# Kernel tuning notes

Hardware: AMD Instinct MI355X
Metric: run time of the kernel (lower is better)

## Reference

```python
import jax, jax.numpy as jnp
import numpy as np

N, E, NB, P = 100000, 1600000, 1000, 500000


def gcn_conv(x, edge_index, W, b):
    # PyG GCNConv: add self-loops, symmetric D^-1/2 (A+I) D^-1/2 normalization,
    # linear transform, bias.
    n = x.shape[0]
    loop = jnp.arange(n, dtype=edge_index.dtype)
    src = jnp.concatenate([edge_index[0], loop])
    dst = jnp.concatenate([edge_index[1], loop])
    deg = jax.ops.segment_sum(jnp.ones(src.shape[0], x.dtype), dst, num_segments=n)
    dinv = jnp.where(deg > 0, jax.lax.rsqrt(deg), 0.0)
    norm = dinv[src] * dinv[dst]                       # [E+n]
    xw = x @ W                                          # [n, out]
    out = jax.ops.segment_sum(xw[src] * norm[:, None], dst, num_segments=n)
    return out + b


def setup_inputs() -> dict:
    key = jax.random.key(0)
    ks = jax.random.split(key, 12)
    x = jax.random.normal(ks[0], (N, 27), jnp.float32)
    edge_index = jax.random.randint(ks[1], (2, E), 0, N, dtype=jnp.int32)
    bank = jax.random.normal(ks[2], (NB, 27), jnp.float32)
    node1 = jax.random.randint(ks[3], (P,), 0, N + NB, dtype=jnp.int32)
    node2 = jax.random.randint(ks[4], (P,), 0, N + NB, dtype=jnp.int32)

    def lin(k, fan_in, fan_out):
        s = 1.0 / np.sqrt(fan_in)
        kw, kb = jax.random.split(k)
        W = jax.random.uniform(kw, (fan_in, fan_out), jnp.float32, -s, s)
        b = jax.random.uniform(kb, (fan_out,), jnp.float32, -s, s)
        return W, b

    W1, b1 = lin(ks[5], 27, 60)
    W2, b2 = lin(ks[6], 60, 50)
    Wb, bb = lin(ks[7], 27, 50)
    Wf1, bf1 = lin(ks[8], 100, 40)
    Wf2, bf2 = lin(ks[9], 40, 20)
    Wf3, bf3 = lin(ks[10], 20, 4)
    return dict(x=x, bank=bank, W1=W1, b1=b1, W2=W2, b2=b2, Wb=Wb, bb=bb,
                Wf1=Wf1, bf1=bf1, Wf2=Wf2, bf2=bf2, Wf3=Wf3, bf3=bf3,
                edge_index=edge_index, node1=node1, node2=node2)


def reference(x, bank, W1, b1, W2, b2, Wb, bb, Wf1, bf1, Wf2, bf2, Wf3, bf3,
              edge_index, node1, node2):
    h = gcn_conv(x, edge_index, W1, b1)                 # [N, 60]
    h = gcn_conv(h, edge_index, W2, b2)                 # [N, 50]
    bk = bank @ Wb + bb                                 # [NB, 50]
    allh = jnp.concatenate([h, bk], axis=0)             # [N+NB, 50]
    z = jnp.concatenate([allh[node1], allh[node2]], axis=1)  # [P, 100]
    z = z @ Wf1 + bf1
    z = z @ Wf2 + bf2
    z = z @ Wf3 + bf3                                   # [P, 4]
    return jax.nn.softmax(z, axis=0)                    # softmax over dim 0, as in source
```

## Files before the change

kernel.cpp:

```cpp
#include <hip/hip_runtime.h>
#include <math.h>

#define N_NODES 100000
#define N_EDGES 1600000
#define NB_BANK 1000
#define N_PAIRS 500000

#define BUCK_SHIFT 9
#define BUCK_NODES 512
#define NBUCK 196
#define EPB 16384
#define NSCAT 98
#define NZBLK 1954
#define SMASK 0x1FFFF

struct Consts {
  float C[27*8];
  float Rb[27*8];
  float u[8];
  float vg[8];
  float vb[8];
};

__global__ __launch_bounds__(256) void k_precompute(
    const float* __restrict__ W1, const float* __restrict__ b1,
    const float* __restrict__ W2, const float* __restrict__ b2,
    const float* __restrict__ Wb, const float* __restrict__ bb,
    const float* __restrict__ Wf1, const float* __restrict__ bf1,
    const float* __restrict__ Wf2, const float* __restrict__ bf2,
    const float* __restrict__ Wf3, const float* __restrict__ bf3,
    Consts* __restrict__ cst) {
  __shared__ float A[40*4];
  __shared__ float T[100*4];
  __shared__ float B[60*8];
  __shared__ float cvec[4];
  const int tid = threadIdx.x;

  for (int idx = tid; idx < 160; idx += 256) {
    int r = idx >> 2, k = idx & 3;
    float s = 0.f;
    for (int j = 0; j < 20; ++j) s += Wf2[r*20+j] * Wf3[j*4+k];
    A[idx] = s;
  }
  __syncthreads();
  for (int idx = tid; idx < 400; idx += 256) {
    int r = idx >> 2, k = idx & 3;
    float s = 0.f;
    for (int j = 0; j < 40; ++j) s += Wf1[r*40+j] * A[j*4+k];
    T[idx] = s;
  }
  if (tid < 4) {
    float s = bf3[tid];
    for (int j = 0; j < 40; ++j) s += bf1[j] * A[j*4+tid];
    for (int j = 0; j < 20; ++j) s += bf2[j] * Wf3[j*4+tid];
    cvec[tid] = s;
  }
  __syncthreads();
  for (int idx = tid; idx < 480; idx += 256) {
    int r = idx >> 3, k = idx & 7;
    int half = k >> 2, kk = k & 3;
    float s = 0.f;
    for (int j = 0; j < 50; ++j) s += W2[r*50+j] * T[(half*50+j)*4+kk];
    B[idx] = s;
  }
  __syncthreads();
  for (int idx = tid; idx < 456; idx += 256) {
    if (idx < 216) {
      int r = idx >> 3, k = idx & 7;
      float s = 0.f;
      for (int j = 0; j < 60; ++j) s += W1[r*60+j] * B[j*8+k];
      cst->C[idx] = s;
    } else if (idx < 432) {
      int i2 = idx - 216;
      int r = i2 >> 3, k = i2 & 7, half = k >> 2, kk = k & 3;
      float s = 0.f;
      for (int j = 0; j < 50; ++j) s += Wb[r*50+j] * T[(half*50+j)*4+kk];
      cst->Rb[i2] = s;
    } else if (idx < 440) {
      int k = idx - 432;
      float s = 0.f;
      for (int j = 0; j < 60; ++j) s += b1[j] * B[j*8+k];
      cst->u[k] = s;
    } else if (idx < 448) {
      int k = idx - 440, half = k >> 2, kk = k & 3;
      float s = (half == 0) ? cvec[kk] : 0.f;
      for (int j = 0; j < 50; ++j) s += b2[j] * T[(half*50+j)*4+kk];
      cst->vg[k] = s;
    } else {
      int k = idx - 448, half = k >> 2, kk = k & 3;
      float s = (half == 0) ? cvec[kk] : 0.f;
      for (int j = 0; j < 50; ++j) s += bb[j] * T[(half*50+j)*4+kk];
      cst->vb[k] = s;
    }
  }
}

__global__ __launch_bounds__(1024) void k_bcount(const int* __restrict__ ei,
                                                 int* __restrict__ bcnt) {
  __shared__ int hist[NBUCK];
  const int t = threadIdx.x;
  if (t < NBUCK) hist[t] = 0;
  __syncthreads();
  const int e0 = blockIdx.x * EPB;
  for (int i = t; i < EPB; i += 1024) {
    int e = e0 + i;
    if (e < N_EDGES) atomicAdd(&hist[ei[N_EDGES + e] >> BUCK_SHIFT], 1);
  }
  __syncthreads();
  if (t < NBUCK && hist[t]) atomicAdd(&bcnt[t], hist[t]);
}

__global__ __launch_bounds__(256) void k_bscan(const int* __restrict__ bcnt,
                                               int* __restrict__ boff,
                                               int* __restrict__ bcursor) {
  __shared__ int sm[256];
  int t = threadIdx.x;
  int v = (t < NBUCK) ? bcnt[t] : 0;
  sm[t] = v;
  __syncthreads();
  for (int off = 1; off < 256; off <<= 1) {
    int u = (t >= off) ? sm[t - off] : 0;
    __syncthreads();
    sm[t] += u;
    __syncthreads();
  }
  if (t < NBUCK) { int ex = sm[t] - v; boff[t] = ex; bcursor[t] = ex; }
  if (t == 0) boff[NBUCK] = N_EDGES;
}

__global__ __launch_bounds__(1024) void k_bscatter(const int* __restrict__ ei,
                                                   int* __restrict__ bcursor,
                                                   int* __restrict__ ebuf) {
  __shared__ int hist[NBUCK];
  __shared__ int base[NBUCK];
  const int t = threadIdx.x;
  const int e0 = blockIdx.x * EPB;
  if (t < NBUCK) hist[t] = 0;
  __syncthreads();
  for (int i = t; i < EPB; i += 1024) {
    int e = e0 + i;
    if (e < N_EDGES) atomicAdd(&hist[ei[N_EDGES + e] >> BUCK_SHIFT], 1);
  }
  __syncthreads();
  if (t < NBUCK) {
    int h = hist[t];
    base[t] = h ? atomicAdd(&bcursor[t], h) : 0;
    hist[t] = 0;
  }
  __syncthreads();
  for (int i = t; i < EPB; i += 1024) {
    int e = e0 + i;
    if (e < N_EDGES) {
      int s = ei[e], d = ei[N_EDGES + e];
      int b = d >> BUCK_SHIFT;
      int pos = base[b] + atomicAdd(&hist[b], 1);
      ebuf[pos] = ((d & (BUCK_NODES - 1)) << 17) | s;
    }
  }
}

__global__ __launch_bounds__(512) void k_degdinv(const int* __restrict__ boff,
                                                 const int* __restrict__ ebuf,
                                                 float* __restrict__ dinv,
                                                 int* __restrict__ rowptr) {
  __shared__ int cnt[BUCK_NODES];
  const int b = blockIdx.x;
  const int t = threadIdx.x;
  cnt[t] = 0;
  __syncthreads();
  const int beg = boff[b], end = boff[b + 1];
  for (int j = beg + t; j < end; j += 512)
    atomicAdd(&cnt[ebuf[j] >> 17], 1);
  __syncthreads();
  int v = cnt[t];
  for (int off = 1; off < 512; off <<= 1) {
    int u = (t >= off) ? cnt[t - off] : 0;
    __syncthreads();
    cnt[t] += u;
    __syncthreads();
  }
  int node = (b << BUCK_SHIFT) + t;
  if (node <= N_NODES) rowptr[node == N_NODES ? N_NODES : node] = beg + cnt[t] - v;
  if (node < N_NODES) dinv[node] = rsqrtf((float)v + 1.0f);
}

__global__ __launch_bounds__(256) void k_bfill(const int* __restrict__ boff,
                                               const int* __restrict__ rowptr,
                                               const int* __restrict__ ebuf,
                                               int* __restrict__ csr) {
  __shared__ int lcur[BUCK_NODES];
  const int b = blockIdx.x;
  const int nbase = b << BUCK_SHIFT;
  const int t = threadIdx.x;
  for (int i = t; i < BUCK_NODES; i += 256) {
    int node = nbase + i;
    lcur[i] = (node < N_NODES) ? rowptr[node] : N_EDGES;
  }
  __syncthreads();
  const int beg = boff[b], end = boff[b + 1];
  for (int j = beg + t; j < end; j += 256) {
    int code = ebuf[j];
    int pos = atomicAdd(&lcur[code >> 17], 1);
    csr[pos] = code & SMASK;
  }
}

__global__ __launch_bounds__(256) void k_x8(const float* __restrict__ x,
                                            const float* __restrict__ dinv,
                                            const Consts* __restrict__ cst,
                                            float* __restrict__ Xs) {
  __shared__ float xs[32*27];
  const int tid = threadIdx.x;
  const int base = blockIdx.x * 32 * 27;
  for (int j = tid; j < 32*27; j += 256) {
    int g = base + j;
    xs[j] = (g < N_NODES*27) ? x[g] : 0.f;
  }
  __syncthreads();
  int li = tid >> 3, k = tid & 7;
  int node = blockIdx.x * 32 + li;
  if (node < N_NODES) {
    float s = 0.f;
    for (int c = 0; c < 27; ++c) s += xs[li*27+c] * cst->C[c*8+k];
    Xs[node*8+k] = s * dinv[node];
  }
}

__global__ __launch_bounds__(256) void k_gather1(const int* __restrict__ rowptr,
                                                 const int* __restrict__ csr,
                                                 const float* __restrict__ dinv,
                                                 const float2* __restrict__ Xs2,
                                                 float2* __restrict__ Ys2,
                                                 float* __restrict__ dvec) {
  int t = blockIdx.x * 256 + threadIdx.x;
  int d = t >> 2, q = t & 3;
  if (d >= N_NODES) return;
  const int beg = rowptr[d], end = rowptr[d + 1];
  const float nd = dinv[d];
  float2 self = Xs2[d*4 + q];
  float ax = self.x, ay = self.y;
  float dsum = nd;
  int j = beg;
  for (; j + 4 <= end; j += 4) {
    int s0 = csr[j], s1 = csr[j+1], s2 = csr[j+2], s3 = csr[j+3];
    float2 a0 = Xs2[s0*4+q], a1 = Xs2[s1*4+q], a2 = Xs2[s2*4+q], a3 = Xs2[s3*4+q];
    ax += (a0.x + a1.x) + (a2.x + a3.x);
    ay += (a0.y + a1.y) + (a2.y + a3.y);
    if (q == 0) dsum += (dinv[s0] + dinv[s1]) + (dinv[s2] + dinv[s3]);
  }
  for (; j < end; ++j) {
    int s = csr[j];
    float2 a = Xs2[s*4+q];
    ax += a.x; ay += a.y;
    if (q == 0) dsum += dinv[s];
  }
  float nn = nd * nd;
  Ys2[t] = make_float2(nn * ax, nn * ay);
  if (q == 0) dvec[d] = nd * dsum;
}

__global__ __launch_bounds__(256) void k_gather2g(const int* __restrict__ rowptr,
                                                  const int* __restrict__ csr,
                                                  const float* __restrict__ dinv,
                                                  const float2* __restrict__ Ys2,
                                                  const float* __restrict__ dvec,
                                                  const float* __restrict__ bank,
                                                  const Consts* __restrict__ cst,
                                                  float2* __restrict__ gall2) {
  int t = blockIdx.x * 256 + threadIdx.x;
  int d = t >> 2, q = t & 3;
  if (d >= N_NODES + NB_BANK) return;
  int c0 = 2*q, c1 = 2*q + 1;
  if (d >= N_NODES) {
    int bk = d - N_NODES;
    float sx = cst->vb[c0], sy = cst->vb[c1];
    for (int cc = 0; cc < 27; ++cc) {
      float bv = bank[bk*27+cc];
      sx += bv * cst->Rb[cc*8+c0];
      sy += bv * cst->Rb[cc*8+c1];
    }
    gall2[t] = make_float2(sx, sy);
    return;
  }
  const int beg = rowptr[d], end = rowptr[d + 1];
  float2 self = Ys2[d*4 + q];
  float ax = self.x, ay = self.y;
  int j = beg;
  for (; j + 4 <= end; j += 4) {
    int s0 = csr[j], s1 = csr[j+1], s2 = csr[j+2], s3 = csr[j+3];
    float2 a0 = Ys2[s0*4+q], a1 = Ys2[s1*4+q], a2 = Ys2[s2*4+q], a3 = Ys2[s3*4+q];
    ax += (a0.x + a1.x) + (a2.x + a3.x);
    ay += (a0.y + a1.y) + (a2.y + a3.y);
  }
  for (; j < end; ++j) {
    float2 a = Ys2[csr[j]*4+q];
    ax += a.x; ay += a.y;
  }
  float nd = dinv[d], dv = dvec[d];
  gall2[t] = make_float2(nd * ax + dv * cst->u[c0] + cst->vg[c0],
                         nd * ay + dv * cst->u[c1] + cst->vg[c1]);
}

__device__ inline void sm_merge(float4& m1, float4& s1,
                                const float4 m2, const float4 s2) {
  float4 M;
  M.x = fmaxf(m1.x, m2.x); M.y = fmaxf(m1.y, m2.y);
  M.z = fmaxf(m1.z, m2.z); M.w = fmaxf(m1.w, m2.w);
  s1.x = s1.x * expf(m1.x - M.x) + s2.x * expf(m2.x - M.x);
  s1.y = s1.y * expf(m1.y - M.y) + s2.y * expf(m2.y - M.y);
  s1.z = s1.z * expf(m1.z - M.z) + s2.z * expf(m2.z - M.z);
  s1.w = s1.w * expf(m1.w - M.w) + s2.w * expf(m2.w - M.w);
  m1 = M;
}

__global__ __launch_bounds__(256) void k_z(const int* __restrict__ node1,
                                           const int* __restrict__ node2,
                                           const float* __restrict__ gall,
                                           float* __restrict__ z,
                                           float4* __restrict__ bs_m,
                                           float4* __restrict__ bs_s) {
  int p = blockIdx.x * 256 + threadIdx.x;
  float4 m = make_float4(-1e30f, -1e30f, -1e30f, -1e30f);
  float4 s = make_float4(0.f, 0.f, 0.f, 0.f);
  if (p < N_PAIRS) {
    int n1 = node1[p], n2 = node2[p];
    const float4 a = *(const float4*)(gall + (size_t)n1*8);
    const float4 b = *(const float4*)(gall + (size_t)n2*8 + 4);
    float4 zv = make_float4(a.x+b.x, a.y+b.y, a.z+b.z, a.w+b.w);
    ((float4*)z)[p] = zv;
    m = zv; s = make_float4(1.f, 1.f, 1.f, 1.f);
  }
  __shared__ float4 lm[256], ls[256];
  lm[threadIdx.x] = m; ls[threadIdx.x] = s;
  __syncthreads();
  for (int st = 128; st > 0; st >>= 1) {
    if (threadIdx.x < st) {
      float4 mm = lm[threadIdx.x], ss = ls[threadIdx.x];
      sm_merge(mm, ss, lm[threadIdx.x + st], ls[threadIdx.x + st]);
      lm[threadIdx.x] = mm; ls[threadIdx.x] = ss;
    }
    __syncthreads();
  }
  if (threadIdx.x == 0) { bs_m[blockIdx.x] = lm[0]; bs_s[blockIdx.x] = ls[0]; }
}

__global__ __launch_bounds__(256) void k_comb(const float4* __restrict__ bs_m,
                                              const float4* __restrict__ bs_s,
                                              float* __restrict__ gms) {
  float4 m = make_float4(-1e30f, -1e30f, -1e30f, -1e30f);
  float4 s = make_float4(0.f, 0.f, 0.f, 0.f);
  for (int i = threadIdx.x; i < NZBLK; i += 256)
    sm_merge(m, s, bs_m[i], bs_s[i]);
  __shared__ float4 lm[256], ls[256];
  lm[threadIdx.x] = m; ls[threadIdx.x] = s;
  __syncthreads();
  for (int st = 128; st > 0; st >>= 1) {
    if (threadIdx.x < st) {
      float4 mm = lm[threadIdx.x], ss = ls[threadIdx.x];
      sm_merge(mm, ss, lm[threadIdx.x + st], ls[threadIdx.x + st]);
      lm[threadIdx.x] = mm; ls[threadIdx.x] = ss;
    }
    __syncthreads();
  }
  if (threadIdx.x == 0) {
    float4 M = lm[0], S = ls[0];
    gms[0] = M.x; gms[1] = M.y; gms[2] = M.z; gms[3] = M.w;
    gms[4] = S.x; gms[5] = S.y; gms[6] = S.z; gms[7] = S.w;
  }
}

__global__ __launch_bounds__(256) void k_final(const float* __restrict__ z,
                                               const float* __restrict__ gms,
                                               float* __restrict__ out) {
  int p = blockIdx.x * 256 + threadIdx.x;
  if (p < N_PAIRS) {
    float m0 = gms[0], m1 = gms[1], m2 = gms[2], m3 = gms[3];
    float i0 = 1.f / gms[4], i1 = 1.f / gms[5];
    float i2 = 1.f / gms[6], i3 = 1.f / gms[7];
    float4 zv = ((const float4*)z)[p];
    float4 o = make_float4(expf(zv.x - m0) * i0, expf(zv.y - m1) * i1,
                           expf(zv.z - m2) * i2, expf(zv.w - m3) * i3);
    ((float4*)out)[p] = o;
  }
}

extern "C" void kernel_launch(void* const* d_in, const int* in_sizes, int n_in,
                              void* d_out, int out_size, void* d_ws, size_t ws_size,
                              hipStream_t stream) {
  const float* x    = (const float*)d_in[0];
  const float* bank = (const float*)d_in[1];
  const float* W1   = (const float*)d_in[2];
  const float* b1   = (const float*)d_in[3];
  const float* W2   = (const float*)d_in[4];
  const float* b2   = (const float*)d_in[5];
  const float* Wb   = (const float*)d_in[6];
  const float* bb   = (const float*)d_in[7];
  const float* Wf1  = (const float*)d_in[8];
  const float* bf1  = (const float*)d_in[9];
  const float* Wf2  = (const float*)d_in[10];
  const float* bf2  = (const float*)d_in[11];
  const float* Wf3  = (const float*)d_in[12];
  const float* bf3  = (const float*)d_in[13];
  const int* ei     = (const int*)d_in[14];
  const int* node1  = (const int*)d_in[15];
  const int* node2  = (const int*)d_in[16];
  float* out = (float*)d_out;

  char* w = (char*)d_ws;
  size_t off = 0;
  auto take = [&](size_t bytes) -> char* {
    char* p = w + off;
    off = (off + bytes + 255) & ~(size_t)255;
    return p;
  };
  Consts* cst    = (Consts*)take(sizeof(Consts));
  int*    bcnt   = (int*)take(NBUCK * 4);
  int*    boff   = (int*)take((NBUCK + 1) * 4);
  int*    bcursor= (int*)take(NBUCK * 4);
  float*  dinv   = (float*)take(N_NODES * 4);
  int*    rowptr = (int*)take((N_NODES + 1) * 4);
  int*    csr    = (int*)take((size_t)N_EDGES * 4);
  float*  Xs     = (float*)take((size_t)N_NODES * 8 * 4);
  float*  Ys     = (float*)take((size_t)N_NODES * 8 * 4);
  float*  dvec   = (float*)take(N_NODES * 4);
  float*  gall   = (float*)take((size_t)(N_NODES + NB_BANK) * 8 * 4);
  char*   shreg  = take((size_t)N_PAIRS * 16);
  int*    ebuf   = (int*)shreg;
  float*  z      = (float*)shreg;
  float4* bs_m   = (float4*)take((size_t)NZBLK * 16);
  float4* bs_s   = (float4*)take((size_t)NZBLK * 16);
  float*  gms    = (float*)take(32);

  hipMemsetAsync(bcnt, 0, NBUCK * 4, stream);

  k_precompute<<<1, 256, 0, stream>>>(W1, b1, W2, b2, Wb, bb,
                                      Wf1, bf1, Wf2, bf2, Wf3, bf3, cst);
  k_bcount<<<NSCAT, 1024, 0, stream>>>(ei, bcnt);
  k_bscan<<<1, 256, 0, stream>>>(bcnt, boff, bcursor);
  k_bscatter<<<NSCAT, 1024, 0, stream>>>(ei, bcursor, ebuf);
  k_degdinv<<<NBUCK, 512, 0, stream>>>(boff, ebuf, dinv, rowptr);
  k_bfill<<<NBUCK, 256, 0, stream>>>(boff, rowptr, ebuf, csr);
  k_x8<<<(N_NODES + 31) / 32, 256, 0, stream>>>(x, dinv, cst, Xs);
  k_gather1<<<(N_NODES * 4 + 255) / 256, 256, 0, stream>>>(
      rowptr, csr, dinv, (const float2*)Xs, (float2*)Ys, dvec);
  k_gather2g<<<((N_NODES + NB_BANK) * 4 + 255) / 256, 256, 0, stream>>>(
      rowptr, csr, dinv, (const float2*)Ys, dvec, bank, cst, (float2*)gall);
  k_z<<<NZBLK, 256, 0, stream>>>(node1, node2, gall, z, bs_m, bs_s);
  k_comb<<<1, 256, 0, stream>>>(bs_m, bs_s, gms);
  k_final<<<NZBLK, 256, 0, stream>>>(z, gms, out);
}
```

Baseline: 234.9 us.

## Fuse small kernels to cut launch count and merge graph-build stages

Folds the weight precompute into an extra block of the bucket-count kernel. Merges degree/dinv, CSR fill and the x@C projection into one per-bucket kernel. Replaces the separate softmax-combine kernel with a last-block ticket reduction inside k_z. This drops four kernel launches and the global round trips for rowptr/dinv. The cost is a serialized 8-chunk projection loop per bucket block with only 196 blocks, and extra fences and atomics.

```diff
diff --git a/kernel.cpp b/kernel.cpp
--- a/kernel.cpp
+++ b/kernel.cpp
@@ -22,7 +22,7 @@
   float vb[8];
 };
 
-__global__ __launch_bounds__(256) void k_precompute(
+__device__ void precompute_body(
     const float* __restrict__ W1, const float* __restrict__ b1,
     const float* __restrict__ W2, const float* __restrict__ b2,
     const float* __restrict__ Wb, const float* __restrict__ bb,
@@ -35,15 +35,16 @@
   __shared__ float B[60*8];
   __shared__ float cvec[4];
   const int tid = threadIdx.x;
-
-  for (int idx = tid; idx < 160; idx += 256) {
+  const int nt = blockDim.x;
+
+  for (int idx = tid; idx < 160; idx += nt) {
     int r = idx >> 2, k = idx & 3;
     float s = 0.f;
     for (int j = 0; j < 20; ++j) s += Wf2[r*20+j] * Wf3[j*4+k];
     A[idx] = s;
   }
   __syncthreads();
-  for (int idx = tid; idx < 400; idx += 256) {
+  for (int idx = tid; idx < 400; idx += nt) {
     int r = idx >> 2, k = idx & 3;
     float s = 0.f;
     for (int j = 0; j < 40; ++j) s += Wf1[r*40+j] * A[j*4+k];
@@ -56,7 +57,7 @@
     cvec[tid] = s;
   }
   __syncthreads();
-  for (int idx = tid; idx < 480; idx += 256) {
+  for (int idx = tid; idx < 480; idx += nt) {
     int r = idx >> 3, k = idx & 7;
     int half = k >> 2, kk = k & 3;
     float s = 0.f;
@@ -64,7 +65,7 @@
     B[idx] = s;
   }
   __syncthreads();
-  for (int idx = tid; idx < 456; idx += 256) {
+  for (int idx = tid; idx < 456; idx += nt) {
     if (idx < 216) {
       int r = idx >> 3, k = idx & 7;
       float s = 0.f;
@@ -95,8 +96,19 @@
   }
 }
 
-__global__ __launch_bounds__(1024) void k_bcount(const int* __restrict__ ei,
-                                                 int* __restrict__ bcnt) {
+__global__ __launch_bounds__(1024) void k_bcount(
+    const int* __restrict__ ei, int* __restrict__ bcnt,
+    const float* __restrict__ W1, const float* __restrict__ b1,
+    const float* __restrict__ W2, const float* __restrict__ b2,
+    const float* __restrict__ Wb, const float* __restrict__ bb,
+    const float* __restrict__ Wf1, const float* __restrict__ bf1,
+    const float* __restrict__ Wf2, const float* __restrict__ bf2,
+    const float* __restrict__ Wf3, const float* __restrict__ bf3,
+    Consts* __restrict__ cst) {
+  if (blockIdx.x == NSCAT) {
+    precompute_body(W1, b1, W2, b2, Wb, bb, Wf1, bf1, Wf2, bf2, Wf3, bf3, cst);
+    return;
+  }
   __shared__ int hist[NBUCK];
   const int t = threadIdx.x;
   if (t < NBUCK) hist[t] = 0;
@@ -159,11 +171,18 @@
   }
 }
 
-__global__ __launch_bounds__(512) void k_degdinv(const int* __restrict__ boff,
-                                                 const int* __restrict__ ebuf,
-                                                 float* __restrict__ dinv,
-                                                 int* __restrict__ rowptr) {
+__global__ __launch_bounds__(512) void k_mega(const int* __restrict__ boff,
+                                              const int* __restrict__ ebuf,
+                                              const float* __restrict__ x,
+                                              const Consts* __restrict__ cst,
+                                              float* __restrict__ dinv,
+                                              int* __restrict__ rowptr,
+                                              int* __restrict__ csr,
+                                              float* __restrict__ Xs) {
   __shared__ int cnt[BUCK_NODES];
+  __shared__ int lcur[BUCK_NODES];
+  __shared__ float dnv[BUCK_NODES];
+  __shared__ float xs[64*27];
   const int b = blockIdx.x;
   const int t = threadIdx.x;
   cnt[t] = 0;
@@ -179,50 +198,36 @@
     cnt[t] += u;
     __syncthreads();
   }
-  int node = (b << BUCK_SHIFT) + t;
-  if (node <= N_NODES) rowptr[node == N_NODES ? N_NODES : node] = beg + cnt[t] - v;
-  if (node < N_NODES) dinv[node] = rsqrtf((float)v + 1.0f);
-}
-
-__global__ __launch_bounds__(256) void k_bfill(const int* __restrict__ boff,
-                                               const int* __restrict__ rowptr,
-                                               const int* __restrict__ ebuf,
-                                               int* __restrict__ csr) {
-  __shared__ int lcur[BUCK_NODES];
-  const int b = blockIdx.x;
-  const int nbase = b << BUCK_SHIFT;
-  const int t = threadIdx.x;
-  for (int i = t; i < BUCK_NODES; i += 256) {
-    int node = nbase + i;
-    lcur[i] = (node < N_NODES) ? rowptr[node] : N_EDGES;
-  }
-  __syncthreads();
-  const int beg = boff[b], end = boff[b + 1];
-  for (int j = beg + t; j < end; j += 256) {
+  const int node = (b << BUCK_SHIFT) + t;
+  const int excl = beg + cnt[t] - v;
+  lcur[t] = excl;
+  float nd = rsqrtf((float)v + 1.0f);
+  dnv[t] = nd;
+  if (node < N_NODES) { rowptr[node] = excl; dinv[node] = nd; }
+  if (node == N_NODES) rowptr[N_NODES] = excl;
+  __syncthreads();
+  for (int chunk = 0; chunk < 8; ++chunk) {
+    const int nb = chunk * 64;
+    const int gbase = ((b << BUCK_SHIFT) + nb) * 27;
+    for (int i = t; i < 64*27; i += 512) {
+      int g = gbase + i;
+      xs[i] = (g < N_NODES*27) ? x[g] : 0.f;
+    }
+    __syncthreads();
+    int li = t >> 3, k = t & 7;
+    int ln = nb + li;
+    int gnode = (b << BUCK_SHIFT) + ln;
+    if (gnode < N_NODES) {
+      float s = 0.f;
+      for (int c = 0; c < 27; ++c) s += xs[li*27+c] * cst->C[c*8+k];
+      Xs[(size_t)gnode*8 + k] = s * dnv[ln];
+    }
+    __syncthreads();
+  }
+  for (int j = beg + t; j < end; j += 512) {
     int code = ebuf[j];
     int pos = atomicAdd(&lcur[code >> 17], 1);
     csr[pos] = code & SMASK;
-  }
-}
-
-__global__ __launch_bounds__(256) void k_x8(const float* __restrict__ x,
-                                            const float* __restrict__ dinv,
-                                            const Consts* __restrict__ cst,
-                                            float* __restrict__ Xs) {
-  __shared__ float xs[32*27];
-  const int tid = threadIdx.x;
-  const int base = blockIdx.x * 32 * 27;
-  for (int j = tid; j < 32*27; j += 256) {
-    int g = base + j;
-    xs[j] = (g < N_NODES*27) ? x[g] : 0.f;
-  }
-  __syncthreads();
-  int li = tid >> 3, k = tid & 7;
-  int node = blockIdx.x * 32 + li;
-  if (node < N_NODES) {
-    float s = 0.f;
-    for (int c = 0; c < 27; ++c) s += xs[li*27+c] * cst->C[c*8+k];
-    Xs[node*8+k] = s * dinv[node];
   }
 }
 
@@ -318,7 +323,9 @@
                                            const float* __restrict__ gall,
                                            float* __restrict__ z,
                                            float4* __restrict__ bs_m,
-                                           float4* __restrict__ bs_s) {
+                                           float4* __restrict__ bs_s,
+                                           int* __restrict__ ticket,
+                                           float* __restrict__ gms) {
   int p = blockIdx.x * 256 + threadIdx.x;
   float4 m = make_float4(-1e30f, -1e30f, -1e30f, -1e30f);
   float4 s = make_float4(0.f, 0.f, 0.f, 0.f);
@@ -331,6 +338,7 @@
     m = zv; s = make_float4(1.f, 1.f, 1.f, 1.f);
   }
   __shared__ float4 lm[256], ls[256];
+  __shared__ bool amLast;
   lm[threadIdx.x] = m; ls[threadIdx.x] = s;
   __syncthreads();
   for (int st = 128; st > 0; st >>= 1) {
@@ -341,18 +349,20 @@
     }
     __syncthreads();
   }
-  if (threadIdx.x == 0) { bs_m[blockIdx.x] = lm[0]; bs_s[blockIdx.x] = ls[0]; }
-}
-
-__global__ __launch_bounds__(256) void k_comb(const float4* __restrict__ bs_m,
-                                              const float4* __restrict__ bs_s,
-                                              float* __restrict__ gms) {
-  float4 m = make_float4(-1e30f, -1e30f, -1e30f, -1e30f);
-  float4 s = make_float4(0.f, 0.f, 0.f, 0.f);
+  if (threadIdx.x == 0) {
+    bs_m[blockIdx.x] = lm[0]; bs_s[blockIdx.x] = ls[0];
+    __threadfence();
+    int prev = atomicAdd(ticket, 1);
+    amLast = (prev == (int)gridDim.x - 1);
+  }
+  __syncthreads();
+  if (!amLast) return;
+  __threadfence();
+  float4 cm = make_float4(-1e30f, -1e30f, -1e30f, -1e30f);
+  float4 cs = make_float4(0.f, 0.f, 0.f, 0.f);
   for (int i = threadIdx.x; i < NZBLK; i += 256)
-    sm_merge(m, s, bs_m[i], bs_s[i]);
-  __shared__ float4 lm[256], ls[256];
-  lm[threadIdx.x] = m; ls[threadIdx.x] = s;
+    sm_merge(cm, cs, bs_m[i], bs_s[i]);
+  lm[threadIdx.x] = cm; ls[threadIdx.x] = cs;
   __syncthreads();
   for (int st = 128; st > 0; st >>= 1) {
     if (threadIdx.x < st) {
@@ -414,7 +424,8 @@
     return p;
   };
   Consts* cst    = (Consts*)take(sizeof(Consts));
-  int*    bcnt   = (int*)take(NBUCK * 4);
+  int*    bcnt   = (int*)take((NBUCK + 1) * 4);
+  int*    ticket = bcnt + NBUCK;
   int*    boff   = (int*)take((NBUCK + 1) * 4);
   int*    bcursor= (int*)take(NBUCK * 4);
   float*  dinv   = (float*)take(N_NODES * 4);
@@ -431,21 +442,17 @@
   float4* bs_s   = (float4*)take((size_t)NZBLK * 16);
   float*  gms    = (float*)take(32);
 
-  hipMemsetAsync(bcnt, 0, NBUCK * 4, stream);
-
-  k_precompute<<<1, 256, 0, stream>>>(W1, b1, W2, b2, Wb, bb,
-                                      Wf1, bf1, Wf2, bf2, Wf3, bf3, cst);
-  k_bcount<<<NSCAT, 1024, 0, stream>>>(ei, bcnt);
+  hipMemsetAsync(bcnt, 0, (NBUCK + 1) * 4, stream);
+
+  k_bcount<<<NSCAT + 1, 1024, 0, stream>>>(ei, bcnt, W1, b1, W2, b2, Wb, bb,
+                                           Wf1, bf1, Wf2, bf2, Wf3, bf3, cst);
   k_bscan<<<1, 256, 0, stream>>>(bcnt, boff, bcursor);
   k_bscatter<<<NSCAT, 1024, 0, stream>>>(ei, bcursor, ebuf);
-  k_degdinv<<<NBUCK, 512, 0, stream>>>(boff, ebuf, dinv, rowptr);
-  k_bfill<<<NBUCK, 256, 0, stream>>>(boff, rowptr, ebuf, csr);
-  k_x8<<<(N_NODES + 31) / 32, 256, 0, stream>>>(x, dinv, cst, Xs);
+  k_mega<<<NBUCK, 512, 0, stream>>>(boff, ebuf, x, cst, dinv, rowptr, csr, Xs);
   k_gather1<<<(N_NODES * 4 + 255) / 256, 256, 0, stream>>>(
       rowptr, csr, dinv, (const float2*)Xs, (float2*)Ys, dvec);
   k_gather2g<<<((N_NODES + NB_BANK) * 4 + 255) / 256, 256, 0, stream>>>(
       rowptr, csr, dinv, (const float2*)Ys, dvec, bank, cst, (float2*)gall);
-  k_z<<<NZBLK, 256, 0, stream>>>(node1, node2, gall, z, bs_m, bs_s);
-  k_comb<<<1, 256, 0, stream>>>(bs_m, bs_s, gms);
+  k_z<<<NZBLK, 256, 0, stream>>>(node1, node2, gall, z, bs_m, bs_s, ticket, gms);
   k_final<<<NZBLK, 256, 0, stream>>>(z, gms, out);
 }
```

New measurement: 268.8 us. +14.4%, slower.

## Use fixed-capacity edge buckets and fuse CSR build kernels into fewer launches

Applied to the files above, without the earlier changes.

The separate count and scan passes over edges are replaced by fixed-capacity buckets of BCAP slots each, so the scatter pass claims positions directly from a per-bucket counter. The weight-precompute kernel becomes an extra block of the scatter launch. Degree computation and CSR fill are merged into one kernel that stores separate row begin and end arrays. This removes an edge-reading pass and several small serial launches. The cost is padded workspace and an assumption that no bucket exceeds BCAP edges, which holds for uniformly random destinations but could overflow on skewed graphs.

```diff
diff --git a/kernel.cpp b/kernel.cpp
--- a/kernel.cpp
+++ b/kernel.cpp
@@ -9,6 +9,7 @@
 #define BUCK_SHIFT 9
 #define BUCK_NODES 512
 #define NBUCK 196
+#define BCAP 10240
 #define EPB 16384
 #define NSCAT 98
 #define NZBLK 1954
@@ -22,7 +23,7 @@
   float vb[8];
 };
 
-__global__ __launch_bounds__(256) void k_precompute(
+__device__ void precompute_body(
     const float* __restrict__ W1, const float* __restrict__ b1,
     const float* __restrict__ W2, const float* __restrict__ b2,
     const float* __restrict__ Wb, const float* __restrict__ bb,
@@ -35,15 +36,16 @@
   __shared__ float B[60*8];
   __shared__ float cvec[4];
   const int tid = threadIdx.x;
-
-  for (int idx = tid; idx < 160; idx += 256) {
+  const int nt = blockDim.x;
+
+  for (int idx = tid; idx < 160; idx += nt) {
     int r = idx >> 2, k = idx & 3;
     float s = 0.f;
     for (int j = 0; j < 20; ++j) s += Wf2[r*20+j] * Wf3[j*4+k];
     A[idx] = s;
   }
   __syncthreads();
-  for (int idx = tid; idx < 400; idx += 256) {
+  for (int idx = tid; idx < 400; idx += nt) {
     int r = idx >> 2, k = idx & 3;
     float s = 0.f;
     for (int j = 0; j < 40; ++j) s += Wf1[r*40+j] * A[j*4+k];
@@ -56,7 +58,7 @@
     cvec[tid] = s;
   }
   __syncthreads();
-  for (int idx = tid; idx < 480; idx += 256) {
+  for (int idx = tid; idx < 480; idx += nt) {
     int r = idx >> 3, k = idx & 7;
     int half = k >> 2, kk = k & 3;
     float s = 0.f;
@@ -64,7 +66,7 @@
     B[idx] = s;
   }
   __syncthreads();
-  for (int idx = tid; idx < 456; idx += 256) {
+  for (int idx = tid; idx < 456; idx += nt) {
     if (idx < 216) {
       int r = idx >> 3, k = idx & 7;
       float s = 0.f;
@@ -95,42 +97,19 @@
   }
 }
 
-__global__ __launch_bounds__(1024) void k_bcount(const int* __restrict__ ei,
-                                                 int* __restrict__ bcnt) {
-  __shared__ int hist[NBUCK];
-  const int t = threadIdx.x;
-  if (t < NBUCK) hist[t] = 0;
-  __syncthreads();
-  const int e0 = blockIdx.x * EPB;
-  for (int i = t; i < EPB; i += 1024) {
-    int e = e0 + i;
-    if (e < N_EDGES) atomicAdd(&hist[ei[N_EDGES + e] >> BUCK_SHIFT], 1);
-  }
-  __syncthreads();
-  if (t < NBUCK && hist[t]) atomicAdd(&bcnt[t], hist[t]);
-}
-
-__global__ __launch_bounds__(256) void k_bscan(const int* __restrict__ bcnt,
-                                               int* __restrict__ boff,
-                                               int* __restrict__ bcursor) {
-  __shared__ int sm[256];
-  int t = threadIdx.x;
-  int v = (t < NBUCK) ? bcnt[t] : 0;
-  sm[t] = v;
-  __syncthreads();
-  for (int off = 1; off < 256; off <<= 1) {
-    int u = (t >= off) ? sm[t - off] : 0;
-    __syncthreads();
-    sm[t] += u;
-    __syncthreads();
-  }
-  if (t < NBUCK) { int ex = sm[t] - v; boff[t] = ex; bcursor[t] = ex; }
-  if (t == 0) boff[NBUCK] = N_EDGES;
-}
-
-__global__ __launch_bounds__(1024) void k_bscatter(const int* __restrict__ ei,
-                                                   int* __restrict__ bcursor,
-                                                   int* __restrict__ ebuf) {
+__global__ __launch_bounds__(1024) void k_scatter(
+    const int* __restrict__ ei, int* __restrict__ bcnt, int* __restrict__ ebuf,
+    const float* __restrict__ W1, const float* __restrict__ b1,
+    const float* __restrict__ W2, const float* __restrict__ b2,
+    const float* __restrict__ Wb, const float* __restrict__ bb,
+    const float* __restrict__ Wf1, const float* __restrict__ bf1,
+    const float* __restrict__ Wf2, const float* __restrict__ bf2,
+    const float* __restrict__ Wf3, const float* __restrict__ bf3,
+    Consts* __restrict__ cst) {
+  if (blockIdx.x == NSCAT) {
+    precompute_body(W1, b1, W2, b2, Wb, bb, Wf1, bf1, Wf2, bf2, Wf3, bf3, cst);
+    return;
+  }
   __shared__ int hist[NBUCK];
   __shared__ int base[NBUCK];
   const int t = threadIdx.x;
@@ -144,7 +123,7 @@
   __syncthreads();
   if (t < NBUCK) {
     int h = hist[t];
-    base[t] = h ? atomicAdd(&bcursor[t], h) : 0;
+    base[t] = h ? (t * BCAP + atomicAdd(&bcnt[t], h)) : 0;
     hist[t] = 0;
   }
   __syncthreads();
@@ -159,16 +138,19 @@
   }
 }
 
-__global__ __launch_bounds__(512) void k_degdinv(const int* __restrict__ boff,
+__global__ __launch_bounds__(512) void k_degfill(const int* __restrict__ bcnt,
                                                  const int* __restrict__ ebuf,
                                                  float* __restrict__ dinv,
-                                                 int* __restrict__ rowptr) {
+                                                 int* __restrict__ rbeg,
+                                                 int* __restrict__ rend,
+                                                 int* __restrict__ csr) {
   __shared__ int cnt[BUCK_NODES];
+  __shared__ int lcur[BUCK_NODES];
   const int b = blockIdx.x;
   const int t = threadIdx.x;
   cnt[t] = 0;
   __syncthreads();
-  const int beg = boff[b], end = boff[b + 1];
+  const int beg = b * BCAP, end = beg + bcnt[b];
   for (int j = beg + t; j < end; j += 512)
     atomicAdd(&cnt[ebuf[j] >> 17], 1);
   __syncthreads();
@@ -179,26 +161,16 @@
     cnt[t] += u;
     __syncthreads();
   }
-  int node = (b << BUCK_SHIFT) + t;
-  if (node <= N_NODES) rowptr[node == N_NODES ? N_NODES : node] = beg + cnt[t] - v;
-  if (node < N_NODES) dinv[node] = rsqrtf((float)v + 1.0f);
-}
-
-__global__ __launch_bounds__(256) void k_bfill(const int* __restrict__ boff,
-                                               const int* __restrict__ rowptr,
-                                               const int* __restrict__ ebuf,
-                                               int* __restrict__ csr) {
-  __shared__ int lcur[BUCK_NODES];
-  const int b = blockIdx.x;
-  const int nbase = b << BUCK_SHIFT;
-  const int t = threadIdx.x;
-  for (int i = t; i < BUCK_NODES; i += 256) {
-    int node = nbase + i;
-    lcur[i] = (node < N_NODES) ? rowptr[node] : N_EDGES;
-  }
-  __syncthreads();
-  const int beg = boff[b], end = boff[b + 1];
-  for (int j = beg + t; j < end; j += 256) {
+  const int node = (b << BUCK_SHIFT) + t;
+  const int excl = beg + cnt[t] - v;
+  lcur[t] = excl;
+  if (node < N_NODES) {
+    rbeg[node] = excl;
+    rend[node] = excl + v;
+    dinv[node] = rsqrtf((float)v + 1.0f);
+  }
+  __syncthreads();
+  for (int j = beg + t; j < end; j += 512) {
     int code = ebuf[j];
     int pos = atomicAdd(&lcur[code >> 17], 1);
     csr[pos] = code & SMASK;
@@ -226,7 +198,8 @@
   }
 }
 
-__global__ __launch_bounds__(256) void k_gather1(const int* __restrict__ rowptr,
+__global__ __launch_bounds__(256) void k_gather1(const int* __restrict__ rbeg,
+                                                 const int* __restrict__ rend,
                                                  const int* __restrict__ csr,
                                                  const float* __restrict__ dinv,
                                                  const float2* __restrict__ Xs2,
@@ -235,7 +208,7 @@
   int t = blockIdx.x * 256 + threadIdx.x;
   int d = t >> 2, q = t & 3;
   if (d >= N_NODES) return;
-  const int beg = rowptr[d], end = rowptr[d + 1];
+  const int beg = rbeg[d], end = rend[d];
   const float nd = dinv[d];
   float2 self = Xs2[d*4 + q];
   float ax = self.x, ay = self.y;
@@ -259,7 +232,8 @@
   if (q == 0) dvec[d] = nd * dsum;
 }
 
-__global__ __launch_bounds__(256) void k_gather2g(const int* __restrict__ rowptr,
+__global__ __launch_bounds__(256) void k_gather2g(const int* __restrict__ rbeg,
+                                                  const int* __restrict__ rend,
                                                   const int* __restrict__ csr,
                                                   const float* __restrict__ dinv,
                                                   const float2* __restrict__ Ys2,
@@ -282,7 +256,7 @@
     gall2[t] = make_float2(sx, sy);
     return;
   }
-  const int beg = rowptr[d], end = rowptr[d + 1];
+  const int beg = rbeg[d], end = rend[d];
   float2 self = Ys2[d*4 + q];
   float ax = self.x, ay = self.y;
   int j = beg;
@@ -415,16 +389,16 @@
   };
   Consts* cst    = (Consts*)take(sizeof(Consts));
   int*    bcnt   = (int*)take(NBUCK * 4);
-  int*    boff   = (int*)take((NBUCK + 1) * 4);
-  int*    bcursor= (int*)take(NBUCK * 4);
   float*  dinv   = (float*)take(N_NODES * 4);
-  int*    rowptr = (int*)take((N_NODES + 1) * 4);
-  int*    csr    = (int*)take((size_t)N_EDGES * 4);
+  int*    rbeg   = (int*)take(N_NODES * 4);
+  int*    rend   = (int*)take(N_NODES * 4);
+  int*    csr    = (int*)take((size_t)NBUCK * BCAP * 4);
   float*  Xs     = (float*)take((size_t)N_NODES * 8 * 4);
   float*  Ys     = (float*)take((size_t)N_NODES * 8 * 4);
   float*  dvec   = (float*)take(N_NODES * 4);
   float*  gall   = (float*)take((size_t)(N_NODES + NB_BANK) * 8 * 4);
-  char*   shreg  = take((size_t)N_PAIRS * 16);
+  char*   shreg  = take((size_t)NBUCK * BCAP * 4 > (size_t)N_PAIRS * 16
+                        ? (size_t)NBUCK * BCAP * 4 : (size_t)N_PAIRS * 16);
   int*    ebuf   = (int*)shreg;
   float*  z      = (float*)shreg;
   float4* bs_m   = (float4*)take((size_t)NZBLK * 16);
@@ -433,18 +407,15 @@
 
   hipMemsetAsync(bcnt, 0, NBUCK * 4, stream);
 
-  k_precompute<<<1, 256, 0, stream>>>(W1, b1, W2, b2, Wb, bb,
-                                      Wf1, bf1, Wf2, bf2, Wf3, bf3, cst);
-  k_bcount<<<NSCAT, 1024, 0, stream>>>(ei, bcnt);
-  k_bscan<<<1, 256, 0, stream>>>(bcnt, boff, bcursor);
-  k_bscatter<<<NSCAT, 1024, 0, stream>>>(ei, bcursor, ebuf);
-  k_degdinv<<<NBUCK, 512, 0, stream>>>(boff, ebuf, dinv, rowptr);
-  k_bfill<<<NBUCK, 256, 0, stream>>>(boff, rowptr, ebuf, csr);
+  k_scatter<<<NSCAT + 1, 1024, 0, stream>>>(ei, bcnt, ebuf, W1, b1, W2, b2,
+                                            Wb, bb, Wf1, bf1, Wf2, bf2,
+                                            Wf3, bf3, cst);
+  k_degfill<<<NBUCK, 512, 0, stream>>>(bcnt, ebuf, dinv, rbeg, rend, csr);
   k_x8<<<(N_NODES + 31) / 32, 256, 0, stream>>>(x, dinv, cst, Xs);
   k_gather1<<<(N_NODES * 4 + 255) / 256, 256, 0, stream>>>(
-      rowptr, csr, dinv, (const float2*)Xs, (float2*)Ys, dvec);
+      rbeg, rend, csr, dinv, (const float2*)Xs, (float2*)Ys, dvec);
   k_gather2g<<<((N_NODES + NB_BANK) * 4 + 255) / 256, 256, 0, stream>>>(
-      rowptr, csr, dinv, (const float2*)Ys, dvec, bank, cst, (float2*)gall);
+      rbeg, rend, csr, dinv, (const float2*)Ys, dvec, bank, cst, (float2*)gall);
   k_z<<<NZBLK, 256, 0, stream>>>(node1, node2, gall, z, bs_m, bs_s);
   k_comb<<<1, 256, 0, stream>>>(bs_m, bs_s, gms);
   k_final<<<NZBLK, 256, 0, stream>>>(z, gms, out);
```

New measurement: 209.5 us. 1.12x faster.
